# Performance work log

Measured on AMD Instinct MI355X. Metric: run time of the kernel, lower is better.

The kernel has to match this reference:

```python
import jax, jax.numpy as jnp
import numpy as np

B, N_RIGIDS, N_RES = 16, 8192, 2048
C_FRAME, C_S, N_AA = 384, 384, 21
EPS = 1e-5


def setup_inputs() -> dict:
    key = jax.random.key(0)
    ks = jax.random.split(key, 8)
    rigids_embed_flat = jax.random.normal(ks[0], (B, N_RIGIDS, C_FRAME), dtype=jnp.float32)
    rigids_to_res_idx = jax.random.randint(ks[1], (B, N_RIGIDS), 0, N_RES, dtype=jnp.int64)
    rigids_mask = jnp.ones((B, N_RIGIDS), dtype=jnp.float32)
    out = jax.random.normal(ks[2], (B, N_RES, C_S), dtype=jnp.float32)
    # params
    ln_g = jnp.ones((C_FRAME,), dtype=jnp.float32)
    ln_b = jnp.zeros((C_FRAME,), dtype=jnp.float32)
    W_su = jax.random.normal(ks[3], (C_FRAME, C_S), dtype=jnp.float32) / np.sqrt(C_FRAME)
    b_su = jnp.zeros((C_S,), dtype=jnp.float32)
    W_out = jax.random.normal(ks[4], (C_S, N_AA), dtype=jnp.float32) / np.sqrt(C_S)
    b_out = jnp.zeros((N_AA,), dtype=jnp.float32)
    return {
        "rigids_embed_flat": rigids_embed_flat,
        "rigids_to_res_idx": rigids_to_res_idx,
        "rigids_mask": rigids_mask,
        "out": out,
        "ln_g": ln_g, "ln_b": ln_b,
        "W_su": W_su, "b_su": b_su,
        "W_out": W_out, "b_out": b_out,
    }


def _layernorm(x, g, b):
    mu = jnp.mean(x, axis=-1, keepdims=True)
    var = jnp.mean(jnp.square(x - mu), axis=-1, keepdims=True)
    return (x - mu) * jax.lax.rsqrt(var + EPS) * g + b


def reference(rigids_embed_flat, rigids_to_res_idx, rigids_mask, out,
              ln_g, ln_b, W_su, b_su, W_out, b_out):
    # 1) LayerNorm over frame channel dim
    x = _layernorm(rigids_embed_flat, ln_g, ln_b)            # [B, N_rigids, c_frame]
    # 2) project frame embed -> c_s and mask invalid frames
    y = (jnp.einsum("bnf,fs->bns", x, W_su) + b_su) * rigids_mask[..., None]
    # 3) scatter-add masked frame contributions into per-residue slots
    seq_embed = jax.vmap(lambda o, yy, ii: o.at[ii].add(yy))(out, y, rigids_to_res_idx)  # [B, N_res, c_s]
    # 4) final projection to amino-acid logits
    return jnp.einsum("brs,sa->bra", seq_embed, W_out) + b_out  # [B, N_res, n_aa]
```

## Files before the change

kernel.cpp:

```cpp
#include <hip/hip_runtime.h>

#define BATCH 16
#define N_RIGIDS 8192
#define N_RES 2048
#define C_FRAME 384
#define C_S 384
#define N_AA 21
#define Z_PAD 24
#define EPS 1e-5f

#define N_RIG_TOT (BATCH * N_RIGIDS)
#define N_ROWS    (BATCH * N_RES)

#define WC_OFF 0
#define GC_OFF 8192
#define CS_OFF 16384
#define B2_OFF 16448
#define Z_OFF  65536
#define HIST_OFF (Z_OFF + N_RIG_TOT * Z_PAD)
#define OFFS_OFF (HIST_OFF + N_ROWS)
#define CUR_OFF  (OFFS_OFF + N_ROWS)
#define BKT_OFF  (CUR_OFF + N_ROWS)

__global__ void precompute_wc(const float* __restrict__ W_su,
                              const float* __restrict__ W_out,
                              const float* __restrict__ ln_g,
                              float* __restrict__ ws) {
    int t = blockIdx.x * blockDim.x + threadIdx.x;
    if (t >= C_FRAME * N_AA) return;
    int f = t / N_AA, a = t % N_AA;
    const float* wrow = W_su + f * C_S;
    float acc = 0.f;
    for (int s = 0; s < C_S; ++s) acc += wrow[s] * W_out[s * N_AA + a];
    ws[WC_OFF + t] = acc;
    ws[GC_OFF + t] = ln_g[f] * acc;
}

__global__ void precompute_bias(const float* __restrict__ ln_b,
                                const float* __restrict__ b_su,
                                const float* __restrict__ W_out,
                                float* __restrict__ ws) {
    int a = threadIdx.x;
    if (a >= N_AA) return;
    float cs = 0.f, b2 = 0.f;
    for (int f = 0; f < C_FRAME; ++f) {
        cs += ws[GC_OFF + f * N_AA + a];
        b2 += ln_b[f] * ws[WC_OFF + f * N_AA + a];
    }
    for (int s = 0; s < C_S; ++s) b2 += b_su[s] * W_out[s * N_AA + a];
    ws[CS_OFF + a] = cs;
    ws[B2_OFF + a] = b2;
}

__global__ void __launch_bounds__(256) zcompute(const float* __restrict__ embed,
                                                const int* __restrict__ idx,
                                                const float* __restrict__ mask,
                                                const float* __restrict__ ws,
                                                float* __restrict__ z,
                                                int* __restrict__ hist) {
    __shared__ float lds[256 * 33];
    const int tid = threadIdx.x;
    const int t = blockIdx.x * 256 + tid;
    const float* __restrict__ Gc = ws + GC_OFF;
    float d[N_AA];
#pragma unroll
    for (int a = 0; a < N_AA; ++a) d[a] = 0.f;
    float sum = 0.f, sumsq = 0.f;

    for (int ch = 0; ch < C_FRAME; ch += 32) {
        __syncthreads();
        const float4* gbase = (const float4*)(embed + (size_t)blockIdx.x * (256 * C_FRAME) + ch);
#pragma unroll
        for (int k = 0; k < 8; ++k) {
            int f4 = tid + 256 * k;
            int r = f4 >> 3, c4 = f4 & 7;
            float4 v = gbase[r * 96 + c4];
            float* p = lds + r * 33 + c4 * 4;
            p[0] = v.x; p[1] = v.y; p[2] = v.z; p[3] = v.w;
        }
        __syncthreads();
        const float* row = lds + tid * 33;
        const float* g = Gc + ch * N_AA;
#pragma unroll 4
        for (int c = 0; c < 32; ++c) {
            float x = row[c];
            sum += x; sumsq += x * x;
#pragma unroll
            for (int a = 0; a < N_AA; ++a) d[a] += x * g[c * N_AA + a];
        }
    }

    float mu  = sum * (1.f / C_FRAME);
    float var = sumsq * (1.f / C_FRAME) - mu * mu;
    float inv = rsqrtf(var + EPS);
    float m = mask[t];
    int res = idx[t];
    int b = t >> 13;
    const float* cs = ws + CS_OFF;
    const float* b2 = ws + B2_OFF;
    float* zr = z + (size_t)t * Z_PAD;
#pragma unroll
    for (int a = 0; a < N_AA; ++a) zr[a] = m * (inv * (d[a] - mu * cs[a]) + b2[a]);
    zr[21] = 0.f; zr[22] = 0.f; zr[23] = 0.f;
    atomicAdd(hist + (b << 11) + res, 1);
}

__global__ void __launch_bounds__(1024) scan_kernel(const int* __restrict__ hist,
                                                    int* __restrict__ offs,
                                                    int* __restrict__ cursor) {
    __shared__ int wtot[16];
    int t = threadIdx.x;
    int lane = t & 63, w = t >> 6;
    int base = t * 32;
    int s = 0;
    for (int i = 0; i < 32; ++i) s += hist[base + i];
    int x = s;
    for (int dlt = 1; dlt < 64; dlt <<= 1) { int v = __shfl_up(x, dlt); if (lane >= dlt) x += v; }
    if (lane == 63) wtot[w] = x;
    __syncthreads();
    if (t < 16) {
        int y = wtot[t];
        for (int dlt = 1; dlt < 16; dlt <<= 1) { int v = __shfl_up(y, dlt); if (t >= dlt) y += v; }
        wtot[t] = y;
    }
    __syncthreads();
    int run = x - s + (w > 0 ? wtot[w - 1] : 0);
    for (int i = 0; i < 32; ++i) {
        int h = hist[base + i];
        offs[base + i] = run;
        cursor[base + i] = run;
        run += h;
    }
}

__global__ void __launch_bounds__(256) bucketfill(const int* __restrict__ idx,
                                                  int* __restrict__ cursor,
                                                  int* __restrict__ bucket) {
    int t = blockIdx.x * 256 + threadIdx.x;
    int b = t >> 13;
    int g = (b << 11) + idx[t];
    int slot = atomicAdd(cursor + g, 1);
    bucket[slot] = t;
}

__global__ void __launch_bounds__(256) final_gather(const float* __restrict__ out_in,
                                                    const float* __restrict__ W_out,
                                                    const float* __restrict__ b_out,
                                                    const float* __restrict__ z,
                                                    const int* __restrict__ offs,
                                                    const int* __restrict__ hist,
                                                    const int* __restrict__ bucket,
                                                    float* __restrict__ logits) {
    __shared__ float lds[256 * 33];
    const int tid = threadIdx.x;
    const int g = blockIdx.x * 256 + tid;
    float acc[N_AA];
#pragma unroll
    for (int a = 0; a < N_AA; ++a) acc[a] = b_out[a];

    for (int ch = 0; ch < C_S; ch += 32) {
        __syncthreads();
        const float4* gbase = (const float4*)(out_in + (size_t)blockIdx.x * (256 * C_S) + ch);
#pragma unroll
        for (int k = 0; k < 8; ++k) {
            int f4 = tid + 256 * k;
            int r = f4 >> 3, c4 = f4 & 7;
            float4 v = gbase[r * 96 + c4];
            float* p = lds + r * 33 + c4 * 4;
            p[0] = v.x; p[1] = v.y; p[2] = v.z; p[3] = v.w;
        }
        __syncthreads();
        const float* row = lds + tid * 33;
        const float* w = W_out + ch * N_AA;
#pragma unroll 4
        for (int c = 0; c < 32; ++c) {
            float x = row[c];
#pragma unroll
            for (int a = 0; a < N_AA; ++a) acc[a] += x * w[c * N_AA + a];
        }
    }

    int start = offs[g], cnt = hist[g];
    for (int i = 0; i < cnt; ++i) {
        int n = bucket[start + i];
        const float4* zr = (const float4*)(z + (size_t)n * Z_PAD);
        float4 z0 = zr[0], z1 = zr[1], z2 = zr[2], z3 = zr[3], z4 = zr[4];
        float  z5 = ((const float*)zr)[20];
        acc[0] += z0.x; acc[1] += z0.y; acc[2] += z0.z; acc[3] += z0.w;
        acc[4] += z1.x; acc[5] += z1.y; acc[6] += z1.z; acc[7] += z1.w;
        acc[8] += z2.x; acc[9] += z2.y; acc[10] += z2.z; acc[11] += z2.w;
        acc[12] += z3.x; acc[13] += z3.y; acc[14] += z3.z; acc[15] += z3.w;
        acc[16] += z4.x; acc[17] += z4.y; acc[18] += z4.z; acc[19] += z4.w;
        acc[20] += z5;
    }
    float* o = logits + (size_t)g * N_AA;
#pragma unroll
    for (int a = 0; a < N_AA; ++a) o[a] = acc[a];
}

extern "C" void kernel_launch(void* const* d_in, const int* in_sizes, int n_in,
                              void* d_out, int out_size, void* d_ws, size_t ws_size,
                              hipStream_t stream) {
    const float* embed  = (const float*)d_in[0];
    const int*   idx    = (const int*)d_in[1];
    const float* mask   = (const float*)d_in[2];
    const float* out_in = (const float*)d_in[3];
    const float* ln_g   = (const float*)d_in[4];
    const float* ln_b   = (const float*)d_in[5];
    const float* W_su   = (const float*)d_in[6];
    const float* b_su   = (const float*)d_in[7];
    const float* W_out  = (const float*)d_in[8];
    const float* b_out  = (const float*)d_in[9];
    float* logits = (float*)d_out;
    float* ws = (float*)d_ws;
    float* z      = ws + Z_OFF;
    int*   hist   = (int*)(ws + HIST_OFF);
    int*   offs   = (int*)(ws + OFFS_OFF);
    int*   cursor = (int*)(ws + CUR_OFF);
    int*   bucket = (int*)(ws + BKT_OFF);

    hipLaunchKernelGGL(precompute_wc, dim3((C_FRAME * N_AA + 255) / 256), dim3(256), 0, stream,
                       W_su, W_out, ln_g, ws);
    hipLaunchKernelGGL(precompute_bias, dim3(1), dim3(64), 0, stream,
                       ln_b, b_su, W_out, ws);
    hipMemsetAsync(hist, 0, N_ROWS * sizeof(int), stream);
    hipLaunchKernelGGL(zcompute, dim3(N_RIG_TOT / 256), dim3(256), 0, stream,
                       embed, idx, mask, ws, z, hist);
    hipLaunchKernelGGL(scan_kernel, dim3(1), dim3(1024), 0, stream,
                       hist, offs, cursor);
    hipLaunchKernelGGL(bucketfill, dim3(N_RIG_TOT / 256), dim3(256), 0, stream,
                       idx, cursor, bucket);
    hipLaunchKernelGGL(final_gather, dim3(N_ROWS / 256), dim3(256), 0, stream,
                       out_in, W_out, b_out, z, offs, hist, bucket, logits);
}
```

Measured before the change: 489.0 us.

## Double-buffer LDS staging, shrink blocks to 128, fuse precompute kernels

The zcompute and final_gather kernels now prefetch the next 32-channel chunk into registers while computing on the current LDS buffer, using two LDS buffers, and launch 128-thread blocks instead of 256. The two weight-precompute kernels are merged into one kernel with one block per output column and a wave-shuffle reduction, which removes a launch and the serial bias loop. zcompute also writes z with float4 stores. The aim is to hide global load latency and raise block-level parallelism, at the cost of extra registers for the prefetch buffer, which may lower occupancy.

```diff
diff --git a/kernel.cpp b/kernel.cpp
--- a/kernel.cpp
+++ b/kernel.cpp
@@ -12,81 +12,112 @@
 #define N_RIG_TOT (BATCH * N_RIGIDS)
 #define N_ROWS    (BATCH * N_RES)
 
-#define WC_OFF 0
-#define GC_OFF 8192
-#define CS_OFF 16384
-#define B2_OFF 16448
-#define Z_OFF  65536
+#define GC_OFF 0
+#define CS_OFF 8192
+#define B2_OFF 8256
+#define Z_OFF  16384
 #define HIST_OFF (Z_OFF + N_RIG_TOT * Z_PAD)
 #define OFFS_OFF (HIST_OFF + N_ROWS)
 #define CUR_OFF  (OFFS_OFF + N_ROWS)
 #define BKT_OFF  (CUR_OFF + N_ROWS)
 
-__global__ void precompute_wc(const float* __restrict__ W_su,
-                              const float* __restrict__ W_out,
-                              const float* __restrict__ ln_g,
-                              float* __restrict__ ws) {
-    int t = blockIdx.x * blockDim.x + threadIdx.x;
-    if (t >= C_FRAME * N_AA) return;
-    int f = t / N_AA, a = t % N_AA;
-    const float* wrow = W_su + f * C_S;
-    float acc = 0.f;
-    for (int s = 0; s < C_S; ++s) acc += wrow[s] * W_out[s * N_AA + a];
-    ws[WC_OFF + t] = acc;
-    ws[GC_OFF + t] = ln_g[f] * acc;
-}
-
-__global__ void precompute_bias(const float* __restrict__ ln_b,
-                                const float* __restrict__ b_su,
-                                const float* __restrict__ W_out,
-                                float* __restrict__ ws) {
-    int a = threadIdx.x;
-    if (a >= N_AA) return;
-    float cs = 0.f, b2 = 0.f;
-    for (int f = 0; f < C_FRAME; ++f) {
-        cs += ws[GC_OFF + f * N_AA + a];
-        b2 += ln_b[f] * ws[WC_OFF + f * N_AA + a];
-    }
-    for (int s = 0; s < C_S; ++s) b2 += b_su[s] * W_out[s * N_AA + a];
-    ws[CS_OFF + a] = cs;
-    ws[B2_OFF + a] = b2;
-}
-
-__global__ void __launch_bounds__(256) zcompute(const float* __restrict__ embed,
+__global__ void __launch_bounds__(384) precompute_fused(const float* __restrict__ W_su,
+                                                        const float* __restrict__ W_out,
+                                                        const float* __restrict__ ln_g,
+                                                        const float* __restrict__ ln_b,
+                                                        const float* __restrict__ b_su,
+                                                        float* __restrict__ ws) {
+    __shared__ float sg[6], sb[6];
+    const int a = blockIdx.x;
+    const int f = threadIdx.x;
+    const float4* wrow = (const float4*)(W_su + (size_t)f * C_S);
+    float wc = 0.f;
+    for (int j = 0; j < C_S / 4; ++j) {
+        float4 v = wrow[j];
+        wc += v.x * W_out[(4 * j + 0) * N_AA + a];
+        wc += v.y * W_out[(4 * j + 1) * N_AA + a];
+        wc += v.z * W_out[(4 * j + 2) * N_AA + a];
+        wc += v.w * W_out[(4 * j + 3) * N_AA + a];
+    }
+    float gval = ln_g[f] * wc;
+    ws[GC_OFF + f * N_AA + a] = gval;
+    float bval = ln_b[f] * wc + b_su[f] * W_out[f * N_AA + a];
+    float g = gval, b = bval;
+#pragma unroll
+    for (int off = 32; off >= 1; off >>= 1) {
+        g += __shfl_xor(g, off);
+        b += __shfl_xor(b, off);
+    }
+    int lane = f & 63, w = f >> 6;
+    if (lane == 0) { sg[w] = g; sb[w] = b; }
+    __syncthreads();
+    if (f == 0) {
+        float cs = 0.f, b2 = 0.f;
+#pragma unroll
+        for (int i = 0; i < 6; ++i) { cs += sg[i]; b2 += sb[i]; }
+        ws[CS_OFF + a] = cs;
+        ws[B2_OFF + a] = b2;
+    }
+}
+
+__global__ void __launch_bounds__(128) zcompute(const float* __restrict__ embed,
                                                 const int* __restrict__ idx,
                                                 const float* __restrict__ mask,
                                                 const float* __restrict__ ws,
                                                 float* __restrict__ z,
                                                 int* __restrict__ hist) {
-    __shared__ float lds[256 * 33];
+    __shared__ float lds[2][128 * 33];
     const int tid = threadIdx.x;
-    const int t = blockIdx.x * 256 + tid;
+    const int t = blockIdx.x * 128 + tid;
     const float* __restrict__ Gc = ws + GC_OFF;
+    const float4* gb = (const float4*)(embed + (size_t)blockIdx.x * (128 * C_FRAME));
+    const int r0 = (tid) >> 3, c0 = (tid) & 7;
+    const int r1 = (tid + 128) >> 3, c1 = (tid + 128) & 7;
+    float4 buf[8];
     float d[N_AA];
 #pragma unroll
     for (int a = 0; a < N_AA; ++a) d[a] = 0.f;
     float sum = 0.f, sumsq = 0.f;
 
-    for (int ch = 0; ch < C_FRAME; ch += 32) {
-        __syncthreads();
-        const float4* gbase = (const float4*)(embed + (size_t)blockIdx.x * (256 * C_FRAME) + ch);
-#pragma unroll
-        for (int k = 0; k < 8; ++k) {
-            int f4 = tid + 256 * k;
-            int r = f4 >> 3, c4 = f4 & 7;
-            float4 v = gbase[r * 96 + c4];
-            float* p = lds + r * 33 + c4 * 4;
-            p[0] = v.x; p[1] = v.y; p[2] = v.z; p[3] = v.w;
-        }
-        __syncthreads();
-        const float* row = lds + tid * 33;
-        const float* g = Gc + ch * N_AA;
+#pragma unroll
+    for (int k = 0; k < 8; ++k) {
+        int f4 = tid + 128 * k;
+        buf[k] = gb[(f4 >> 3) * 96 + (f4 & 7)];
+    }
+#pragma unroll
+    for (int k = 0; k < 8; ++k) {
+        int f4 = tid + 128 * k;
+        float* p = &lds[0][(f4 >> 3) * 33 + (f4 & 7) * 4];
+        p[0] = buf[k].x; p[1] = buf[k].y; p[2] = buf[k].z; p[3] = buf[k].w;
+    }
+    __syncthreads();
+
+    for (int c = 0; c < 12; ++c) {
+        if (c + 1 < 12) {
+            const float4* gn = gb + (c + 1) * 8;
+#pragma unroll
+            for (int k = 0; k < 8; ++k) {
+                int f4 = tid + 128 * k;
+                buf[k] = gn[(f4 >> 3) * 96 + (f4 & 7)];
+            }
+        }
+        const float* row = &lds[c & 1][tid * 33];
+        const float* g = Gc + (c * 32) * N_AA;
 #pragma unroll 4
-        for (int c = 0; c < 32; ++c) {
-            float x = row[c];
+        for (int cc = 0; cc < 32; ++cc) {
+            float x = row[cc];
             sum += x; sumsq += x * x;
 #pragma unroll
-            for (int a = 0; a < N_AA; ++a) d[a] += x * g[c * N_AA + a];
+            for (int a = 0; a < N_AA; ++a) d[a] += x * g[cc * N_AA + a];
+        }
+        if (c + 1 < 12) {
+#pragma unroll
+            for (int k = 0; k < 8; ++k) {
+                int f4 = tid + 128 * k;
+                float* p = &lds[(c + 1) & 1][(f4 >> 3) * 33 + (f4 & 7) * 4];
+                p[0] = buf[k].x; p[1] = buf[k].y; p[2] = buf[k].z; p[3] = buf[k].w;
+            }
+            __syncthreads();
         }
     }
 
@@ -98,11 +129,18 @@
     int b = t >> 13;
     const float* cs = ws + CS_OFF;
     const float* b2 = ws + B2_OFF;
-    float* zr = z + (size_t)t * Z_PAD;
-#pragma unroll
-    for (int a = 0; a < N_AA; ++a) zr[a] = m * (inv * (d[a] - mu * cs[a]) + b2[a]);
-    zr[21] = 0.f; zr[22] = 0.f; zr[23] = 0.f;
+    float v[N_AA];
+#pragma unroll
+    for (int a = 0; a < N_AA; ++a) v[a] = m * (inv * (d[a] - mu * cs[a]) + b2[a]);
+    float4* zr4 = (float4*)(z + (size_t)t * Z_PAD);
+    zr4[0] = make_float4(v[0], v[1], v[2], v[3]);
+    zr4[1] = make_float4(v[4], v[5], v[6], v[7]);
+    zr4[2] = make_float4(v[8], v[9], v[10], v[11]);
+    zr4[3] = make_float4(v[12], v[13], v[14], v[15]);
+    zr4[4] = make_float4(v[16], v[17], v[18], v[19]);
+    z[(size_t)t * Z_PAD + 20] = v[20];
     atomicAdd(hist + (b << 11) + res, 1);
+    (void)r0; (void)c0; (void)r1; (void)c1;
 }
 
 __global__ void __launch_bounds__(1024) scan_kernel(const int* __restrict__ hist,
@@ -143,7 +181,7 @@
     bucket[slot] = t;
 }
 
-__global__ void __launch_bounds__(256) final_gather(const float* __restrict__ out_in,
+__global__ void __launch_bounds__(128) final_gather(const float* __restrict__ out_in,
                                                     const float* __restrict__ W_out,
                                                     const float* __restrict__ b_out,
                                                     const float* __restrict__ z,
@@ -151,36 +189,57 @@
                                                     const int* __restrict__ hist,
                                                     const int* __restrict__ bucket,
                                                     float* __restrict__ logits) {
-    __shared__ float lds[256 * 33];
+    __shared__ float lds[2][128 * 33];
     const int tid = threadIdx.x;
-    const int g = blockIdx.x * 256 + tid;
+    const int gidx = blockIdx.x * 128 + tid;
+    const float4* gb = (const float4*)(out_in + (size_t)blockIdx.x * (128 * C_S));
+    float4 buf[8];
     float acc[N_AA];
 #pragma unroll
     for (int a = 0; a < N_AA; ++a) acc[a] = b_out[a];
 
-    for (int ch = 0; ch < C_S; ch += 32) {
-        __syncthreads();
-        const float4* gbase = (const float4*)(out_in + (size_t)blockIdx.x * (256 * C_S) + ch);
-#pragma unroll
-        for (int k = 0; k < 8; ++k) {
-            int f4 = tid + 256 * k;
-            int r = f4 >> 3, c4 = f4 & 7;
-            float4 v = gbase[r * 96 + c4];
-            float* p = lds + r * 33 + c4 * 4;
-            p[0] = v.x; p[1] = v.y; p[2] = v.z; p[3] = v.w;
-        }
-        __syncthreads();
-        const float* row = lds + tid * 33;
-        const float* w = W_out + ch * N_AA;
+#pragma unroll
+    for (int k = 0; k < 8; ++k) {
+        int f4 = tid + 128 * k;
+        buf[k] = gb[(f4 >> 3) * 96 + (f4 & 7)];
+    }
+#pragma unroll
+    for (int k = 0; k < 8; ++k) {
+        int f4 = tid + 128 * k;
+        float* p = &lds[0][(f4 >> 3) * 33 + (f4 & 7) * 4];
+        p[0] = buf[k].x; p[1] = buf[k].y; p[2] = buf[k].z; p[3] = buf[k].w;
+    }
+    __syncthreads();
+
+    for (int c = 0; c < 12; ++c) {
+        if (c + 1 < 12) {
+            const float4* gn = gb + (c + 1) * 8;
+#pragma unroll
+            for (int k = 0; k < 8; ++k) {
+                int f4 = tid + 128 * k;
+                buf[k] = gn[(f4 >> 3) * 96 + (f4 & 7)];
+            }
+        }
+        const float* row = &lds[c & 1][tid * 33];
+        const float* w = W_out + (c * 32) * N_AA;
 #pragma unroll 4
-        for (int c = 0; c < 32; ++c) {
-            float x = row[c];
-#pragma unroll
-            for (int a = 0; a < N_AA; ++a) acc[a] += x * w[c * N_AA + a];
-        }
-    }
-
-    int start = offs[g], cnt = hist[g];
+        for (int cc = 0; cc < 32; ++cc) {
+            float x = row[cc];
+#pragma unroll
+            for (int a = 0; a < N_AA; ++a) acc[a] += x * w[cc * N_AA + a];
+        }
+        if (c + 1 < 12) {
+#pragma unroll
+            for (int k = 0; k < 8; ++k) {
+                int f4 = tid + 128 * k;
+                float* p = &lds[(c + 1) & 1][(f4 >> 3) * 33 + (f4 & 7) * 4];
+                p[0] = buf[k].x; p[1] = buf[k].y; p[2] = buf[k].z; p[3] = buf[k].w;
+            }
+            __syncthreads();
+        }
+    }
+
+    int start = offs[gidx], cnt = hist[gidx];
     for (int i = 0; i < cnt; ++i) {
         int n = bucket[start + i];
         const float4* zr = (const float4*)(z + (size_t)n * Z_PAD);
@@ -193,7 +252,7 @@
         acc[16] += z4.x; acc[17] += z4.y; acc[18] += z4.z; acc[19] += z4.w;
         acc[20] += z5;
     }
-    float* o = logits + (size_t)g * N_AA;
+    float* o = logits + (size_t)gidx * N_AA;
 #pragma unroll
     for (int a = 0; a < N_AA; ++a) o[a] = acc[a];
 }
@@ -219,17 +278,15 @@
     int*   cursor = (int*)(ws + CUR_OFF);
     int*   bucket = (int*)(ws + BKT_OFF);
 
-    hipLaunchKernelGGL(precompute_wc, dim3((C_FRAME * N_AA + 255) / 256), dim3(256), 0, stream,
-                       W_su, W_out, ln_g, ws);
-    hipLaunchKernelGGL(precompute_bias, dim3(1), dim3(64), 0, stream,
-                       ln_b, b_su, W_out, ws);
     hipMemsetAsync(hist, 0, N_ROWS * sizeof(int), stream);
-    hipLaunchKernelGGL(zcompute, dim3(N_RIG_TOT / 256), dim3(256), 0, stream,
+    hipLaunchKernelGGL(precompute_fused, dim3(N_AA), dim3(384), 0, stream,
+                       W_su, W_out, ln_g, ln_b, b_su, ws);
+    hipLaunchKernelGGL(zcompute, dim3(N_RIG_TOT / 128), dim3(128), 0, stream,
                        embed, idx, mask, ws, z, hist);
     hipLaunchKernelGGL(scan_kernel, dim3(1), dim3(1024), 0, stream,
                        hist, offs, cursor);
     hipLaunchKernelGGL(bucketfill, dim3(N_RIG_TOT / 256), dim3(256), 0, stream,
                        idx, cursor, bucket);
-    hipLaunchKernelGGL(final_gather, dim3(N_ROWS / 256), dim3(256), 0, stream,
+    hipLaunchKernelGGL(final_gather, dim3(N_ROWS / 128), dim3(128), 0, stream,
                        out_in, W_out, b_out, z, offs, hist, bucket, logits);
 }
```

Result: faster. 459.9 us (-6.0%).
